# Kernel tuning notes

Measured on AMD Instinct MI355X. Metric: run time of the kernel, lower is better.

The kernel has to match this reference:

```python
import jax, jax.numpy as jnp
import numpy as np

D_MODEL = 512
NHEAD = 8
D_HEAD = D_MODEL // NHEAD
SCALE = D_HEAD ** -0.5
EPS = 1e-8


def setup_inputs() -> dict:
    key = jax.random.key(0)
    ks = jax.random.split(key, 12)
    B, N = 4, 2048
    s = D_MODEL ** -0.5
    return {
        "Q_input": jax.random.normal(ks[0], (B, N, D_MODEL), jnp.float32),
        "KV_input": jax.random.normal(ks[1], (B, N, D_MODEL), jnp.float32),
        "SC": jax.random.uniform(ks[2], (B, N, N), jnp.float32),
        "Wq_w": jax.random.normal(ks[3], (D_MODEL, D_MODEL), jnp.float32) * s,
        "Wq_b": jnp.zeros((D_MODEL,), jnp.float32),
        "Wk_w": jax.random.normal(ks[4], (D_MODEL, D_MODEL), jnp.float32) * s,
        "Wk_b": jnp.zeros((D_MODEL,), jnp.float32),
        "Wv_w": jax.random.normal(ks[5], (D_MODEL, D_MODEL), jnp.float32) * s,
        "Wv_b": jnp.zeros((D_MODEL,), jnp.float32),
        "gate_w": jax.random.normal(ks[6], (), jnp.float32),
        "gate_b": jnp.zeros((), jnp.float32),
        "out_w": jax.random.normal(ks[7], (D_MODEL, D_MODEL), jnp.float32) * s,
        "out_b": jnp.zeros((D_MODEL,), jnp.float32),
    }


def reference(Q_input, KV_input, SC, Wq_w, Wq_b, Wk_w, Wk_b, Wv_w, Wv_b,
              gate_w, gate_b, out_w, out_b):
    B, N, _ = Q_input.shape
    # projections -> [B, H, N, d_head]
    def proj(x, w, b):
        y = x @ w.T + b
        return y.reshape(B, N, NHEAD, D_HEAD).transpose(0, 2, 1, 3)
    Q = proj(Q_input, Wq_w, Wq_b)
    K = proj(KV_input, Wk_w, Wk_b)
    V = proj(KV_input, Wv_w, Wv_b)
    # scores [B, H, N, N]
    scores = jnp.einsum('bhqd,bhkd->bhqk', Q, K) * SCALE
    # per-edge gate: sigmoid(w*SC + b), broadcast over heads
    g = jax.nn.sigmoid(SC * gate_w + gate_b)  # [B, N, N]
    scores = scores + jnp.log(g + EPS)[:, None, :, :]
    attn = jax.nn.softmax(scores, axis=-1)
    out = jnp.einsum('bhqk,bhkd->bhqd', attn, V)
    out = out.transpose(0, 2, 1, 3).reshape(B, N, D_MODEL)
    return out @ out_w.T + out_b
```

## Files before the change

kernel.cpp:

```cpp
#include <hip/hip_runtime.h>

typedef unsigned short u16;
typedef unsigned int u32;
typedef __attribute__((ext_vector_type(4))) float f32x4;
typedef __attribute__((ext_vector_type(8))) short s16x8;
typedef __attribute__((ext_vector_type(4))) u16 u16x4;
typedef __attribute__((ext_vector_type(2))) u32 u32x2;

#define L2E 1.4426950408889634f
#define QSCALE 0.18033688011112042f

__device__ __forceinline__ float bf2f(u16 u) {
    union { u32 i; float f; } v; v.i = ((u32)u) << 16; return v.f;
}
__device__ __forceinline__ u16 f2bf(float f) {
    union { float f; u32 i; } v; v.f = f;
    return (u16)((v.i + 0x7fffu + ((v.i >> 16) & 1u)) >> 16);
}
__device__ __forceinline__ u32 pack_hi(float a, float b) {
    union { float f; u32 i; } x, y; x.f = a; y.f = b;
    return (x.i >> 16) | (y.i & 0xFFFF0000u);
}
__device__ __forceinline__ float bflo(u32 w) {
    union { u32 i; float f; } v; v.i = w << 16; return v.f;
}
__device__ __forceinline__ float bfhi(u32 w) {
    union { u32 i; float f; } v; v.i = w & 0xFFFF0000u; return v.f;
}

__device__ __forceinline__ void gl2lds16(const u16* g, u16* l) {
    __builtin_amdgcn_global_load_lds(
        (const __attribute__((address_space(1))) void*)g,
        (__attribute__((address_space(3))) void*)l, 16, 0, 0);
}

__global__ __launch_bounds__(256) void prep_kernel(
    const float* __restrict__ s0, const float* __restrict__ s1,
    const float* __restrict__ s2, const float* __restrict__ s3,
    const float* __restrict__ s4, const float* __restrict__ s5,
    u16* __restrict__ dst,
    const float* __restrict__ SC, const float* __restrict__ gwp,
    const float* __restrict__ gbp, u16* __restrict__ LGx)
{
    if (blockIdx.x < 9216) {
        int e = (blockIdx.x * 256 + threadIdx.x) * 4;
        const float* src; int off;
        if      (e < 4194304) { src = s0; off = e; }
        else if (e < 8388608) { src = s1; off = e - 4194304; }
        else if (e < 8650752) { src = s2; off = e - 8388608; }
        else if (e < 8912896) { src = s3; off = e - 8650752; }
        else if (e < 9175040) { src = s4; off = e - 8912896; }
        else                  { src = s5; off = e - 9175040; }
        f32x4 f = *(const f32x4*)(src + off);
        u16x4 o;
#pragma unroll
        for (int j = 0; j < 4; ++j) o[j] = f2bf(f[j]);
        *(u16x4*)(dst + e) = o;
    } else {
        const int flat = (blockIdx.x - 9216) * 256 + threadIdx.x;
        const int lane = flat & 63;
        const int kt   = (flat >> 6) & 31;
        const int t16  = (flat >> 11) & 127;
        const int b    = flat >> 18;
        const int l16 = lane & 15, quad = lane >> 4;
        const float tA = -gwp[0] * L2E, tB = -gbp[0] * L2E;
        const float* row = SC + ((size_t)b * 2048 + t16 * 16 + l16) * 2048
                              + kt * 64 + quad * 4;
        __align__(16) u16 tmp[16];
#pragma unroll
        for (int kk = 0; kk < 4; ++kk) {
            f32x4 x = *(const f32x4*)(row + kk * 16);
#pragma unroll
            for (int reg = 0; reg < 4; ++reg) {
                float g = __builtin_amdgcn_rcpf(
                    1.0f + __builtin_amdgcn_exp2f(tA * x[reg] + tB)) + 1e-8f;
                tmp[kk * 4 + reg] = f2bf(__builtin_amdgcn_logf(g));
            }
        }
        u16* d = LGx + (size_t)flat * 16;
        *(uint4*)d       = *(uint4*)tmp;
        *(uint4*)(d + 8) = *(uint4*)(tmp + 8);
    }
}

__device__ __forceinline__ void gemm_core(
    const u16* __restrict__ A, const u16* __restrict__ Bw,
    int m0, int n0, u16* As, u16* Bs, f32x4 acc[4][4])
{
    const int tid = threadIdx.x;
    const int lane = tid & 63, w = tid >> 6;
    const int wm = w >> 1, wn = w & 1;
    const int l16 = lane & 15, quad = lane >> 4;
    const int srow = (lane >> 2), sch = (lane & 3) * 8;
    const f32x4 vzero = {0.f, 0.f, 0.f, 0.f};
#pragma unroll
    for (int i = 0; i < 4; ++i)
#pragma unroll
        for (int j = 0; j < 4; ++j) acc[i][j] = vzero;

#pragma unroll
    for (int j = 0; j < 2; ++j) {
        int row = w * 32 + j * 16 + srow;
        gl2lds16(&A[(size_t)(m0 + row) * 512 + sch], &As[w * 1024 + j * 512]);
        gl2lds16(&Bw[(size_t)(n0 + row) * 512 + sch], &Bs[w * 1024 + j * 512]);
    }
    for (int kt = 0; kt < 16; ++kt) {
        __syncthreads();
        const int cur = (kt & 1) * 4096;
        if (kt < 15) {
            const int nxt = ((kt + 1) & 1) * 4096;
#pragma unroll
            for (int j = 0; j < 2; ++j) {
                int row = w * 32 + j * 16 + srow;
                gl2lds16(&A[(size_t)(m0 + row) * 512 + (kt + 1) * 32 + sch],
                         &As[nxt + w * 1024 + j * 512]);
                gl2lds16(&Bw[(size_t)(n0 + row) * 512 + (kt + 1) * 32 + sch],
                         &Bs[nxt + w * 1024 + j * 512]);
            }
        }
        s16x8 af[4], bfr[4];
#pragma unroll
        for (int mt = 0; mt < 4; ++mt)
            af[mt] = *(const s16x8*)&As[cur + (wm * 64 + mt * 16 + l16) * 32 + quad * 8];
#pragma unroll
        for (int nt = 0; nt < 4; ++nt)
            bfr[nt] = *(const s16x8*)&Bs[cur + (wn * 64 + nt * 16 + l16) * 32 + quad * 8];
#pragma unroll
        for (int mt = 0; mt < 4; ++mt)
#pragma unroll
            for (int nt = 0; nt < 4; ++nt)
                acc[mt][nt] = __builtin_amdgcn_mfma_f32_16x16x32_bf16(
                    af[mt], bfr[nt], acc[mt][nt], 0, 0, 0);
    }
}

__global__ __launch_bounds__(256) void proj_kernel(
    const u16* __restrict__ cQin, const u16* __restrict__ cKV,
    const u16* __restrict__ cW,
    const float* __restrict__ bq, const float* __restrict__ bk,
    const float* __restrict__ bv,
    u16* __restrict__ Qh, u16* __restrict__ Kh, u16* __restrict__ Vt)
{
    __shared__ __align__(16) u16 As[2 * 4096];
    __shared__ __align__(16) u16 Bs[2 * 4096];
    const int job = blockIdx.z;
    const u16* A = (job == 0) ? cQin : cKV;
    const u16* W = cW + (size_t)job * 262144;
    const float* bias = (job == 0) ? bq : (job == 1 ? bk : bv);
    const int m0 = blockIdx.y * 128, n0 = blockIdx.x * 128;
    f32x4 acc[4][4];
    gemm_core(A, W, m0, n0, As, Bs, acc);

    const int tid = threadIdx.x, lane = tid & 63, w = tid >> 6;
    const int wm = w >> 1, wn = w & 1, l16 = lane & 15, quad = lane >> 4;
#pragma unroll
    for (int nt = 0; nt < 4; ++nt) {
        int j = n0 + wn * 64 + nt * 16 + l16;
        float bj = bias[j];
        int h = j >> 6, d = j & 63;
#pragma unroll
        for (int mt = 0; mt < 4; ++mt) {
            int trow = m0 + wm * 64 + mt * 16 + quad * 4;
            int bb = trow >> 11, nn = trow & 2047;
            int bh = bb * 8 + h;
            if (job == 2) {
                u16x4 pv;
#pragma unroll
                for (int reg = 0; reg < 4; ++reg) pv[reg] = f2bf(acc[mt][nt][reg] + bj);
                *(u16x4*)&Vt[(size_t)(bh * 64 + d) * 2048 + nn] = pv;
            } else if (job == 0) {
#pragma unroll
                for (int reg = 0; reg < 4; ++reg)
                    Qh[(size_t)(bh * 2048 + nn + reg) * 64 + d] =
                        f2bf((acc[mt][nt][reg] + bj) * QSCALE);
            } else {
#pragma unroll
                for (int reg = 0; reg < 4; ++reg)
                    Kh[(size_t)(bh * 2048 + nn + reg) * 64 + d] =
                        f2bf(acc[mt][nt][reg] + bj);
            }
        }
    }
}

__global__ __launch_bounds__(512, 4) void attn_kernel(
    const u16* __restrict__ Qh, const u16* __restrict__ Kh,
    const u16* __restrict__ Vt, const u16* __restrict__ LGx,
    u16* __restrict__ Ob)
{
    __shared__ __align__(16) u16 Ks[2][4096];
    __shared__ __align__(16) u16 Vs[2][4096];
    const int tid = threadIdx.x;
    const int w = tid >> 6, lane = tid & 63;
    const int l16 = lane & 15, quad = lane >> 4;
    const int b = blockIdx.z, head = blockIdx.y, qg = blockIdx.x;
    const int bh = b * 8 + head;
    const int q0 = qg * 128 + w * 16;
    const int t16 = qg * 8 + w;
    const u16* Qp = Qh + (size_t)bh * 131072;
    const u16* Kp = Kh + (size_t)bh * 131072;
    const u16* Vp = Vt + (size_t)bh * 131072;
    const u16* LGt = LGx + ((size_t)((b * 128 + t16) * 32) * 64 + lane) * 16;
    const f32x4 vzero = {0.f, 0.f, 0.f, 0.f};
    const s16x8 ones = {0x3F80, 0x3F80, 0x3F80, 0x3F80,
                        0x3F80, 0x3F80, 0x3F80, 0x3F80};

    const int sr = lane >> 3;
    const int scw = ((lane & 7) ^ sr) * 8;
    const int slab = (w & 3) * 16;
    const bool isK = (w < 4);
    const u16* sG0 = isK ? (Kp + (size_t)(slab + sr) * 64 + scw)
                         : (Vp + (size_t)(slab + sr) * 2048 + scw);
    const u16* sG1 = isK ? (Kp + (size_t)(slab + 8 + sr) * 64 + scw)
                         : (Vp + (size_t)(slab + 8 + sr) * 2048 + scw);
    const size_t sAdv = isK ? 4096 : 64;
    u16* sL0 = isK ? &Ks[0][slab * 64] : &Vs[0][slab * 64];
    u16* sL1 = isK ? &Ks[0][(slab + 8) * 64] : &Vs[0][(slab + 8) * 64];

    s16x8 qf[2];
#pragma unroll
    for (int kc = 0; kc < 2; ++kc)
        qf[kc] = *(const s16x8*)&Qp[(size_t)(q0 + l16) * 64 + kc * 32 + quad * 8];
    f32x4 o[4], lacc = vzero;
#pragma unroll
    for (int dn = 0; dn < 4; ++dn) o[dn] = vzero;

    gl2lds16(sG0, sL0);
    gl2lds16(sG1, sL1);

    uint4 lgA = *(const uint4*)LGt;
    uint4 lgB = *(const uint4*)(LGt + 8);

    for (int kt = 0; kt < 32; ++kt) {
        __syncthreads();
        const int cur = kt & 1;
        if (kt < 31) {
            const int nxt = cur ^ 1;
            gl2lds16(sG0 + (size_t)(kt + 1) * sAdv, sL0 + nxt * 4096);
            gl2lds16(sG1 + (size_t)(kt + 1) * sAdv, sL1 + nxt * 4096);
        }
        const u16* Kb = &Ks[cur][0];
        const u16* Vb = &Vs[cur][0];

        f32x4 cin[4];
        {
            const u32 wd[8] = {lgA.x, lgA.y, lgA.z, lgA.w,
                               lgB.x, lgB.y, lgB.z, lgB.w};
#pragma unroll
            for (int kk = 0; kk < 4; ++kk) {
                cin[kk][0] = bflo(wd[kk * 2]);
                cin[kk][1] = bfhi(wd[kk * 2]);
                cin[kk][2] = bflo(wd[kk * 2 + 1]);
                cin[kk][3] = bfhi(wd[kk * 2 + 1]);
            }
        }
        if (kt < 31) {
            lgA = *(const uint4*)(LGt + (size_t)(kt + 1) * 1024);
            lgB = *(const uint4*)(LGt + (size_t)(kt + 1) * 1024 + 8);
        }

        f32x4 st[4];
#pragma unroll
        for (int kc = 0; kc < 2; ++kc) {
            s16x8 kf[4];
#pragma unroll
            for (int kk = 0; kk < 4; ++kk)
                kf[kk] = *(const s16x8*)&Kb[(kk * 16 + l16) * 64 +
                                            ((kc * 4 + quad) ^ (l16 & 7)) * 8];
#pragma unroll
            for (int kk = 0; kk < 4; ++kk)
                st[kk] = __builtin_amdgcn_mfma_f32_16x16x32_bf16(
                    kf[kk], qf[kc], kc == 0 ? cin[kk] : st[kk], 0, 0, 0);
        }

        u32 Pw[4][2];
#pragma unroll
        for (int kk = 0; kk < 4; ++kk) {
            float p0 = __builtin_amdgcn_exp2f(st[kk][0]);
            float p1 = __builtin_amdgcn_exp2f(st[kk][1]);
            float p2 = __builtin_amdgcn_exp2f(st[kk][2]);
            float p3 = __builtin_amdgcn_exp2f(st[kk][3]);
            Pw[kk][0] = pack_hi(p0, p1);
            Pw[kk][1] = pack_hi(p2, p3);
        }

#pragma unroll
        for (int kc = 0; kc < 2; ++kc) {
            union { u32 wrd[4]; s16x8 v; } pu;
#pragma unroll
            for (int i = 0; i < 2; ++i) {
                u32x2 r1 = __builtin_amdgcn_permlane32_swap(
                    Pw[2 * kc][i], Pw[2 * kc + 1][i], false, false);
                u32x2 r2 = __builtin_amdgcn_permlane16_swap(
                    r1[0], r1[1], false, false);
                pu.wrd[i]     = r2[0];
                pu.wrd[2 + i] = r2[1];
            }
            s16x8 pf = pu.v;
            lacc = __builtin_amdgcn_mfma_f32_16x16x32_bf16(pf, ones, lacc, 0, 0, 0);
            s16x8 vf[4];
#pragma unroll
            for (int dn = 0; dn < 4; ++dn)
                vf[dn] = *(const s16x8*)&Vb[(dn * 16 + l16) * 64 +
                                            ((kc * 4 + quad) ^ (l16 & 7)) * 8];
#pragma unroll
            for (int dn = 0; dn < 4; ++dn)
                o[dn] = __builtin_amdgcn_mfma_f32_16x16x32_bf16(
                    pf, vf[dn], o[dn], 0, 0, 0);
        }
    }
#pragma unroll
    for (int reg = 0; reg < 4; ++reg) {
        float inv = __builtin_amdgcn_rcpf(lacc[reg]);
        int trow = b * 2048 + q0 + quad * 4 + reg;
#pragma unroll
        for (int dn = 0; dn < 4; ++dn)
            Ob[(size_t)trow * 512 + head * 64 + dn * 16 + l16] =
                f2bf(o[dn][reg] * inv);
    }
}

__global__ __launch_bounds__(256) void out_kernel(
    const u16* __restrict__ Ob, const u16* __restrict__ cWo,
    const float* __restrict__ bo, float* __restrict__ out)
{
    __shared__ __align__(16) u16 As[2 * 4096];
    __shared__ __align__(16) u16 Bs[2 * 4096];
    const int m0 = blockIdx.y * 128, n0 = blockIdx.x * 128;
    f32x4 acc[4][4];
    gemm_core(Ob, cWo, m0, n0, As, Bs, acc);
    const int tid = threadIdx.x, lane = tid & 63, w = tid >> 6;
    const int wm = w >> 1, wn = w & 1, l16 = lane & 15, quad = lane >> 4;
#pragma unroll
    for (int nt = 0; nt < 4; ++nt) {
        int j = n0 + wn * 64 + nt * 16 + l16;
        float bj = bo[j];
#pragma unroll
        for (int mt = 0; mt < 4; ++mt) {
            int t = m0 + wm * 64 + mt * 16 + quad * 4;
#pragma unroll
            for (int reg = 0; reg < 4; ++reg)
                out[(size_t)(t + reg) * 512 + j] = acc[mt][nt][reg] + bj;
        }
    }
}

extern "C" void kernel_launch(void* const* d_in, const int* in_sizes, int n_in,
                              void* d_out, int out_size, void* d_ws, size_t ws_size,
                              hipStream_t stream)
{
    const float* Qin  = (const float*)d_in[0];
    const float* KVin = (const float*)d_in[1];
    const float* SC   = (const float*)d_in[2];
    const float* Wq   = (const float*)d_in[3];
    const float* bq   = (const float*)d_in[4];
    const float* Wk   = (const float*)d_in[5];
    const float* bk   = (const float*)d_in[6];
    const float* Wv   = (const float*)d_in[7];
    const float* bv   = (const float*)d_in[8];
    const float* gw   = (const float*)d_in[9];
    const float* gb   = (const float*)d_in[10];
    const float* Wo   = (const float*)d_in[11];
    const float* bo   = (const float*)d_in[12];
    float* out = (float*)d_out;

    u16* conv = (u16*)d_ws;
    u16* cQin = conv;
    u16* cKV  = conv + 4194304;
    u16* cW   = conv + 8388608;
    u16* Qh   = conv + 9437184;
    u16* Kh   = Qh + 4194304;
    u16* Vt   = Kh + 4194304;
    u16* Ob   = Vt + 4194304;
    u16* LGx  = Ob + 4194304;

    hipLaunchKernelGGL(prep_kernel, dim3(13312), dim3(256), 0, stream,
                       Qin, KVin, Wq, Wk, Wv, Wo, conv, SC, gw, gb, LGx);
    hipLaunchKernelGGL(proj_kernel, dim3(4, 64, 3), dim3(256), 0, stream,
                       cQin, cKV, cW, bq, bk, bv, Qh, Kh, Vt);
    hipLaunchKernelGGL(attn_kernel, dim3(16, 8, 4), dim3(512), 0, stream,
                       Qh, Kh, Vt, LGx, Ob);
    hipLaunchKernelGGL(out_kernel, dim3(4, 64), dim3(256), 0, stream,
                       Ob, cW + 786432, bo, out);
}
```

Measured before the change: 240.9 us.

## Double attention K/V tile to 128 keys per iteration with new swizzle and setprio

The attention inner loop now processes 128 keys per iteration instead of 64, halving the iteration and barrier count. K/V LDS buffers grow to 8192 elements per stage with a reworked XOR swizzle, and four async global-to-LDS copies are issued per thread. The gate-log loads are prefetched two tiles at a time, and s_setprio raises wave priority around the MFMA section. The larger LDS footprint (64KB per block) may cut occupancy against the launch_bounds(512,4) target.

New measurement: 243.2 us. About the same (+1.0%).

```diff
diff --git a/kernel.cpp b/kernel.cpp
--- a/kernel.cpp
+++ b/kernel.cpp
@@ -188,8 +188,8 @@
     const u16* __restrict__ Vt, const u16* __restrict__ LGx,
     u16* __restrict__ Ob)
 {
-    __shared__ __align__(16) u16 Ks[2][4096];
-    __shared__ __align__(16) u16 Vs[2][4096];
+    __shared__ __align__(16) u16 Ks[2][8192];
+    __shared__ __align__(16) u16 Vs[2][8192];
     const int tid = threadIdx.x;
     const int w = tid >> 6, lane = tid & 63;
     const int l16 = lane & 15, quad = lane >> 4;
@@ -205,87 +205,95 @@
     const s16x8 ones = {0x3F80, 0x3F80, 0x3F80, 0x3F80,
                         0x3F80, 0x3F80, 0x3F80, 0x3F80};
 
-    const int sr = lane >> 3;
-    const int scw = ((lane & 7) ^ sr) * 8;
-    const int slab = (w & 3) * 16;
+    const int s3 = l16 & 7, s2x = s3 & 3, s4x = s3 & 4;
+    const int qsw = (quad ^ s2x) * 8;
+    const int kb0 = l16 * 64 + qsw + s4x * 8;
+    const int kb1 = l16 * 64 + qsw + (4 ^ s4x) * 8;
+    const int vb0 = l16 * 128 + qsw + s4x * 8;
+    const int vb1 = l16 * 128 + qsw + (4 ^ s4x) * 8;
+    const u16* KbL = &Ks[0][0];
+    const u16* VbL = &Vs[0][0];
+
+    const int w4 = w & 3;
     const bool isK = (w < 4);
-    const u16* sG0 = isK ? (Kp + (size_t)(slab + sr) * 64 + scw)
-                         : (Vp + (size_t)(slab + sr) * 2048 + scw);
-    const u16* sG1 = isK ? (Kp + (size_t)(slab + 8 + sr) * 64 + scw)
-                         : (Vp + (size_t)(slab + 8 + sr) * 2048 + scw);
-    const size_t sAdv = isK ? 4096 : 64;
-    u16* sL0 = isK ? &Ks[0][slab * 64] : &Vs[0][slab * 64];
-    u16* sL1 = isK ? &Ks[0][(slab + 8) * 64] : &Vs[0][(slab + 8) * 64];
-
-    s16x8 qf[2];
-#pragma unroll
-    for (int kc = 0; kc < 2; ++kc)
-        qf[kc] = *(const s16x8*)&Qp[(size_t)(q0 + l16) * 64 + kc * 32 + quad * 8];
+    const int srK = lane >> 3, c8 = lane & 7;
+    const int sr4 = lane >> 4, c16 = lane & 15;
+    const u16* sg0 = isK
+        ? (Kp + (size_t)(w4 * 32 + 0 + srK) * 64 + (c8 ^ srK) * 8)
+        : (Vp + (size_t)(w4 * 16 + 0 + sr4) * 2048 + (c16 ^ ((0 + sr4) & 7)) * 8);
+    const u16* sg1 = isK
+        ? (Kp + (size_t)(w4 * 32 + 8 + srK) * 64 + (c8 ^ srK) * 8)
+        : (Vp + (size_t)(w4 * 16 + 4 + sr4) * 2048 + (c16 ^ ((4 + sr4) & 7)) * 8);
+    const u16* sg2 = isK
+        ? (Kp + (size_t)(w4 * 32 + 16 + srK) * 64 + (c8 ^ srK) * 8)
+        : (Vp + (size_t)(w4 * 16 + 8 + sr4) * 2048 + (c16 ^ ((8 + sr4) & 7)) * 8);
+    const u16* sg3 = isK
+        ? (Kp + (size_t)(w4 * 32 + 24 + srK) * 64 + (c8 ^ srK) * 8)
+        : (Vp + (size_t)(w4 * 16 + 12 + sr4) * 2048 + (c16 ^ ((12 + sr4) & 7)) * 8);
+    const size_t sAdv = isK ? 8192 : 128;
+    u16* sd0 = isK ? &Ks[0][(w4 * 32 + 0) * 64]  : &Vs[0][(w4 * 16 + 0) * 128];
+    u16* sd1 = isK ? &Ks[0][(w4 * 32 + 8) * 64]  : &Vs[0][(w4 * 16 + 4) * 128];
+    u16* sd2 = isK ? &Ks[0][(w4 * 32 + 16) * 64] : &Vs[0][(w4 * 16 + 8) * 128];
+    u16* sd3 = isK ? &Ks[0][(w4 * 32 + 24) * 64] : &Vs[0][(w4 * 16 + 12) * 128];
+
+    s16x8 qf0 = *(const s16x8*)&Qp[(size_t)(q0 + l16) * 64 + quad * 8];
+    s16x8 qf1 = *(const s16x8*)&Qp[(size_t)(q0 + l16) * 64 + 32 + quad * 8];
     f32x4 o[4], lacc = vzero;
 #pragma unroll
     for (int dn = 0; dn < 4; ++dn) o[dn] = vzero;
 
-    gl2lds16(sG0, sL0);
-    gl2lds16(sG1, sL1);
-
-    uint4 lgA = *(const uint4*)LGt;
-    uint4 lgB = *(const uint4*)(LGt + 8);
-
-    for (int kt = 0; kt < 32; ++kt) {
+    gl2lds16(sg0, sd0); gl2lds16(sg1, sd1);
+    gl2lds16(sg2, sd2); gl2lds16(sg3, sd3);
+    sg0 += sAdv; sg1 += sAdv; sg2 += sAdv; sg3 += sAdv;
+    uint4 lg0 = *(const uint4*)LGt;
+    uint4 lg1 = *(const uint4*)(LGt + 8);
+    uint4 lg2 = *(const uint4*)(LGt + 1024);
+    uint4 lg3 = *(const uint4*)(LGt + 1032);
+    const u16* lgP = LGt + 2048;
+
+#define QKHALF(LA, LB, PWB, KOFF)                                              \
+    {                                                                          \
+        const u32 wdh[8] = {LA.x, LA.y, LA.z, LA.w, LB.x, LB.y, LB.z, LB.w};   \
+        _Pragma("unroll")                                                      \
+        for (int kk = 0; kk < 4; ++kk) {                                       \
+            f32x4 ci;                                                          \
+            ci[0] = bflo(wdh[kk * 2]);     ci[1] = bfhi(wdh[kk * 2]);          \
+            ci[2] = bflo(wdh[kk * 2 + 1]); ci[3] = bfhi(wdh[kk * 2 + 1]);      \
+            s16x8 ka = *(const s16x8*)(KbL + bo + kb0 + (KOFF + kk) * 1024);   \
+            s16x8 kb = *(const s16x8*)(KbL + bo + kb1 + (KOFF + kk) * 1024);   \
+            f32x4 s = __builtin_amdgcn_mfma_f32_16x16x32_bf16(ka, qf0, ci, 0, 0, 0); \
+            s = __builtin_amdgcn_mfma_f32_16x16x32_bf16(kb, qf1, s, 0, 0, 0);  \
+            float p0 = __builtin_amdgcn_exp2f(s[0]);                           \
+            float p1 = __builtin_amdgcn_exp2f(s[1]);                           \
+            float p2 = __builtin_amdgcn_exp2f(s[2]);                           \
+            float p3 = __builtin_amdgcn_exp2f(s[3]);                           \
+            Pw[PWB + kk][0] = pack_hi(p0, p1);                                 \
+            Pw[PWB + kk][1] = pack_hi(p2, p3);                                 \
+        }                                                                      \
+    }
+
+    for (int kt = 0; kt < 16; ++kt) {
         __syncthreads();
-        const int cur = kt & 1;
-        if (kt < 31) {
-            const int nxt = cur ^ 1;
-            gl2lds16(sG0 + (size_t)(kt + 1) * sAdv, sL0 + nxt * 4096);
-            gl2lds16(sG1 + (size_t)(kt + 1) * sAdv, sL1 + nxt * 4096);
-        }
-        const u16* Kb = &Ks[cur][0];
-        const u16* Vb = &Vs[cur][0];
-
-        f32x4 cin[4];
-        {
-            const u32 wd[8] = {lgA.x, lgA.y, lgA.z, lgA.w,
-                               lgB.x, lgB.y, lgB.z, lgB.w};
-#pragma unroll
-            for (int kk = 0; kk < 4; ++kk) {
-                cin[kk][0] = bflo(wd[kk * 2]);
-                cin[kk][1] = bfhi(wd[kk * 2]);
-                cin[kk][2] = bflo(wd[kk * 2 + 1]);
-                cin[kk][3] = bfhi(wd[kk * 2 + 1]);
-            }
-        }
-        if (kt < 31) {
-            lgA = *(const uint4*)(LGt + (size_t)(kt + 1) * 1024);
-            lgB = *(const uint4*)(LGt + (size_t)(kt + 1) * 1024 + 8);
-        }
-
-        f32x4 st[4];
-#pragma unroll
-        for (int kc = 0; kc < 2; ++kc) {
-            s16x8 kf[4];
-#pragma unroll
-            for (int kk = 0; kk < 4; ++kk)
-                kf[kk] = *(const s16x8*)&Kb[(kk * 16 + l16) * 64 +
-                                            ((kc * 4 + quad) ^ (l16 & 7)) * 8];
-#pragma unroll
-            for (int kk = 0; kk < 4; ++kk)
-                st[kk] = __builtin_amdgcn_mfma_f32_16x16x32_bf16(
-                    kf[kk], qf[kc], kc == 0 ? cin[kk] : st[kk], 0, 0, 0);
-        }
-
-        u32 Pw[4][2];
-#pragma unroll
-        for (int kk = 0; kk < 4; ++kk) {
-            float p0 = __builtin_amdgcn_exp2f(st[kk][0]);
-            float p1 = __builtin_amdgcn_exp2f(st[kk][1]);
-            float p2 = __builtin_amdgcn_exp2f(st[kk][2]);
-            float p3 = __builtin_amdgcn_exp2f(st[kk][3]);
-            Pw[kk][0] = pack_hi(p0, p1);
-            Pw[kk][1] = pack_hi(p2, p3);
-        }
-
-#pragma unroll
-        for (int kc = 0; kc < 2; ++kc) {
+        const int bo = (kt & 1) * 8192;
+        if (kt < 15) {
+            const int bn = 8192 - bo;
+            gl2lds16(sg0, sd0 + bn); gl2lds16(sg1, sd1 + bn);
+            gl2lds16(sg2, sd2 + bn); gl2lds16(sg3, sd3 + bn);
+            sg0 += sAdv; sg1 += sAdv; sg2 += sAdv; sg3 += sAdv;
+        }
+        __builtin_amdgcn_s_setprio(1);
+        u32 Pw[8][2];
+        QKHALF(lg0, lg1, 0, 0);
+        QKHALF(lg2, lg3, 4, 4);
+        if (kt < 15) {
+            lg0 = *(const uint4*)lgP;
+            lg1 = *(const uint4*)(lgP + 8);
+            lg2 = *(const uint4*)(lgP + 1024);
+            lg3 = *(const uint4*)(lgP + 1032);
+            lgP += 2048;
+        }
+#pragma unroll
+        for (int kc = 0; kc < 4; ++kc) {
             union { u32 wrd[4]; s16x8 v; } pu;
 #pragma unroll
             for (int i = 0; i < 2; ++i) {
@@ -298,17 +306,17 @@
             }
             s16x8 pf = pu.v;
             lacc = __builtin_amdgcn_mfma_f32_16x16x32_bf16(pf, ones, lacc, 0, 0, 0);
-            s16x8 vf[4];
-#pragma unroll
-            for (int dn = 0; dn < 4; ++dn)
-                vf[dn] = *(const s16x8*)&Vb[(dn * 16 + l16) * 64 +
-                                            ((kc * 4 + quad) ^ (l16 & 7)) * 8];
-#pragma unroll
-            for (int dn = 0; dn < 4; ++dn)
+            const int vbb = ((kc & 1) ? vb1 : vb0) + (kc >> 1) * 64 + bo;
+#pragma unroll
+            for (int dn = 0; dn < 4; ++dn) {
+                s16x8 vf = *(const s16x8*)(VbL + vbb + dn * 2048);
                 o[dn] = __builtin_amdgcn_mfma_f32_16x16x32_bf16(
-                    pf, vf[dn], o[dn], 0, 0, 0);
-        }
-    }
+                    pf, vf, o[dn], 0, 0, 0);
+            }
+        }
+        __builtin_amdgcn_s_setprio(0);
+    }
+#undef QKHALF
 #pragma unroll
     for (int reg = 0; reg < 4; ++reg) {
         float inv = __builtin_amdgcn_rcpf(lacc[reg]);
```
